# Kernel tuning notes

Hardware: AMD Instinct MI355X
Metric: run time of the kernel (lower is better)

## Reference

```python
import jax, jax.numpy as jnp
import numpy as np

B, S, DIM, HID, NE, TOPK = 2, 2048, 1024, 4096, 8, 2


def setup_inputs() -> dict:
    key = jax.random.key(0)
    ks = jax.random.split(key, 4)
    def init(k, shape, fan_in):
        return jax.random.normal(k, shape, jnp.float32) * (1.0 / np.sqrt(fan_in))
    return {
        "x": jax.random.normal(ks[0], (B, S, DIM), jnp.float32),
        "Wg": init(ks[1], (DIM, NE), DIM),
        "bg": jnp.zeros((NE,), jnp.float32),
        "W1": init(ks[2], (NE, DIM, HID), DIM),
        "b1": jnp.zeros((NE, HID), jnp.float32),
        "W2": init(ks[3], (NE, HID, DIM), HID),
        "b2": jnp.zeros((NE, DIM), jnp.float32),
        "top_k": TOPK,
    }


def reference(x, Wg, bg, W1, b1, W2, b2, top_k):
    Bx, Sx, D = x.shape
    T = Bx * Sx
    xt = x.reshape(T, D)                                   # [T, D] tokens
    # --- router: top-k softmax gating ---
    logits = xt @ Wg + bg                                  # [T, E]
    top_vals, top_idx = jax.lax.top_k(logits, top_k)       # [T, k]
    gate_w = jax.nn.softmax(top_vals, axis=-1)             # renormalized over chosen experts
    num_e = Wg.shape[1]
    # sparse combine weights: zero for non-selected experts
    w = jnp.zeros((T, num_e), xt.dtype).at[jnp.arange(T)[:, None], top_idx].set(gate_w)  # [T, E]
    # --- per-expert FFN (dense grouped-GEMM form) ---
    h = jax.nn.gelu(jnp.einsum('td,edh->eth', xt, W1) + b1[:, None, :])   # [E, T, H]
    y = jnp.einsum('eth,ehd->etd', h, W2) + b2[:, None, :]                # [E, T, D]
    moe_out = jnp.einsum('etd,te->td', y, w)                              # weighted combine
    # --- residual add (MoEBlock.forward: moe_out + skip; norm is unused) ---
    return (moe_out + xt).reshape(Bx, Sx, D)
```

## Files before the change

kernel.cpp:

```cpp
#include <hip/hip_runtime.h>

#define T_TOKENS 4096
#define DIM      1024
#define HID      4096
#define NE       8
#define TOPK     2
#define MAXTILES 72

typedef __attribute__((ext_vector_type(8))) short short8;
typedef __attribute__((ext_vector_type(4))) float f32x4;

__device__ __forceinline__ unsigned short f2bf(float f) {
    unsigned int u = __builtin_bit_cast(unsigned int, f);
    u += 0x7fffu + ((u >> 16) & 1u);
    return (unsigned short)(u >> 16);
}

__device__ __forceinline__ void gload16(const void* g, void* l) {
    __builtin_amdgcn_global_load_lds(
        (const __attribute__((address_space(1))) unsigned int*)g,
        (__attribute__((address_space(3))) unsigned int*)l, 16, 0, 0);
}

__global__ void router_kernel(const float* __restrict__ x, const float* __restrict__ Wg,
                              const float* __restrict__ bg, int* __restrict__ counts,
                              int* __restrict__ rowlist, float* __restrict__ gatelist) {
    const int wid  = threadIdx.x >> 6;
    const int lane = threadIdx.x & 63;
    const int t = blockIdx.x * 4 + wid;
    float acc[NE];
#pragma unroll
    for (int e = 0; e < NE; ++e) acc[e] = 0.f;
    const float* xr = x + (size_t)t * DIM;
    for (int d = lane; d < DIM; d += 64) {
        const float xv = xr[d];
        const float* wr = Wg + (size_t)d * NE;
#pragma unroll
        for (int e = 0; e < NE; ++e) acc[e] += xv * wr[e];
    }
#pragma unroll
    for (int off = 32; off > 0; off >>= 1) {
#pragma unroll
        for (int e = 0; e < NE; ++e) acc[e] += __shfl_xor(acc[e], off);
    }
    if (lane == 0) {
        float lg[NE];
#pragma unroll
        for (int e = 0; e < NE; ++e) lg[e] = acc[e] + bg[e];
        int i1 = 0; float v1 = lg[0];
#pragma unroll
        for (int e = 1; e < NE; ++e) if (lg[e] > v1) { v1 = lg[e]; i1 = e; }
        int i2 = -1; float v2 = -3.4e38f;
#pragma unroll
        for (int e = 0; e < NE; ++e) if (e != i1 && lg[e] > v2) { v2 = lg[e]; i2 = e; }
        const float ex = expf(v2 - v1);
        const float g1 = 1.f / (1.f + ex);
        const float g2 = ex / (1.f + ex);
        int p1 = atomicAdd(&counts[i1], 1);
        rowlist[i1 * T_TOKENS + p1] = t * 2;
        gatelist[i1 * T_TOKENS + p1] = g1;
        int p2 = atomicAdd(&counts[i2], 1);
        rowlist[i2 * T_TOKENS + p2] = t * 2 + 1;
        gatelist[i2 * T_TOKENS + p2] = g2;
    }
}

__global__ void planner_kernel(const int* __restrict__ counts, int* __restrict__ wl1,
                               int* __restrict__ wl2, int* __restrict__ nw) {
    __shared__ int tiles[NE], pref[NE + 1];
    const int tid = threadIdx.x;
    if (tid == 0) {
        int p = 0;
        for (int e = 0; e < NE; ++e) {
            tiles[e] = (counts[e] + 127) >> 7;
            pref[e] = p;
            p += tiles[e];
        }
        pref[NE] = p;
        nw[0] = p * 32;
        nw[1] = p * 16;
    }
    __syncthreads();
    const int n1 = pref[NE] * 32, n2 = pref[NE] * 16;
    for (int i = tid; i < n1; i += 256) {
        int e = 0;
        while (pref[e + 1] * 32 <= i) ++e;
        const int rel = i - pref[e] * 32;
        const int colt = rel / tiles[e];
        const int rt = rel - colt * tiles[e];
        wl1[i] = (e << 16) | (colt << 7) | rt;
    }
    for (int i = tid; i < n2; i += 256) {
        int e = 0;
        while (pref[e + 1] * 16 <= i) ++e;
        const int rel = i - pref[e] * 16;
        const int grp = rel / tiles[e];
        const int rt = rel - grp * tiles[e];
        wl2[i] = (e << 16) | ((grp >> 3) << 13) | ((grp & 7) << 7) | rt;
    }
}

__global__ void conv_bf16_kernel(const float* __restrict__ x, unsigned short* __restrict__ xb) {
    const int i = blockIdx.x * 256 + threadIdx.x;
    const float4 v = ((const float4*)x)[i];
    ushort4 o;
    o.x = f2bf(v.x); o.y = f2bf(v.y); o.z = f2bf(v.z); o.w = f2bf(v.w);
    ((ushort4*)xb)[i] = o;
}

__global__ void init_out_kernel(const float* __restrict__ x, float* __restrict__ out) {
    const int i = blockIdx.x * 256 + threadIdx.x;
    ((float4*)out)[i] = ((const float4*)x)[i];
}

template <int K, int N>
__global__ __launch_bounds__(256) void transconv_kernel(const float* __restrict__ W,
                                                        unsigned short* __restrict__ Wb) {
    const int e  = blockIdx.z;
    const int k0 = blockIdx.y * 64;
    const int nb = blockIdx.x * 64;
    __shared__ unsigned short t[64][72];
    const int tid = threadIdx.x;
    const int r  = tid >> 4;
    const int c4 = (tid & 15) * 4;
    const float* src = W + (size_t)e * K * N + (size_t)(k0 + r) * N + nb + c4;
#pragma unroll
    for (int p = 0; p < 4; ++p) {
        const float4 v = *(const float4*)(src + (size_t)p * 16 * N);
        ushort4 o;
        o.x = f2bf(v.x); o.y = f2bf(v.y); o.z = f2bf(v.z); o.w = f2bf(v.w);
        *(ushort4*)(&t[r + p * 16][c4]) = o;
    }
    __syncthreads();
#pragma unroll
    for (int p = 0; p < 4; ++p) {
        const int n  = (tid >> 4) + p * 16;
        const int kk = (tid & 15) * 4;
        ushort4 o;
        o.x = t[kk][n]; o.y = t[kk + 1][n]; o.z = t[kk + 2][n]; o.w = t[kk + 3][n];
        *(ushort4*)(Wb + (size_t)e * N * K + (size_t)(nb + n) * K + k0 + kk) = o;
    }
}

template <int PHASE, int SPLITK>
__global__ __launch_bounds__(256, 4) void moe_gemm(
    const unsigned short* __restrict__ A, const unsigned short* __restrict__ Wb,
    const float* __restrict__ bias, const int* __restrict__ counts,
    const int* __restrict__ rowlist, const float* __restrict__ gatelist,
    const int* __restrict__ wl, const int* __restrict__ nw,
    unsigned short* __restrict__ h, float* __restrict__ out) {
    constexpr int K = (PHASE == 1) ? DIM : HID;
    constexpr int N = (PHASE == 1) ? HID : DIM;
    constexpr int KC = K / SPLITK;
    constexpr int NT = KC / 64;
    const int nwork = nw[PHASE - 1];
    const int chunk = (nwork + 7) >> 3;
    const int pos = blockIdx.x >> 3;
    if (pos >= chunk) return;
    const int widx = (blockIdx.x & 7) * chunk + pos;
    if (widx >= nwork) return;
    const int w = wl[widx];
    const int e    = (w >> 16) & 7;
    const int kc   = (w >> 13) & 7;
    const int colt = (w >> 7) & 0x3f;
    const int rt   = w & 0x7f;
    const int cnt  = counts[e];
    const int n0   = colt * 128;

    __shared__ __align__(16) unsigned short As[128][64];
    __shared__ __align__(16) unsigned short Bs[128][64];
    __shared__ int rows_s[128];
    __shared__ float gates_s[128];

    const int tid = threadIdx.x;
    if (tid < 128) {
        const int gr = rt * 128 + tid;
        const int src = e * T_TOKENS + ((gr < cnt) ? gr : 0);
        rows_s[tid] = rowlist[src];
        gates_s[tid] = (gr < cnt) ? gatelist[src] : 0.f;
    }
    __syncthreads();

    const int lane = tid & 63;
    const int wv = tid >> 6;

    const int rowin = lane >> 3;
    const int kofs = ((lane & 7) ^ rowin) * 8;
    const unsigned short* sA[4];
    const unsigned short* sB[4];
    int dLds[4];
#pragma unroll
    for (int j = 0; j < 4; ++j) {
        const int r = (wv * 4 + j) * 8 + rowin;
        const int rid = rows_s[r];
        sA[j] = A + (size_t)((PHASE == 1) ? (rid >> 1) : rid) * K + kc * KC + kofs;
        sB[j] = Wb + (size_t)e * N * K + (size_t)(n0 + r) * K + kc * KC + kofs;
        dLds[j] = (wv * 4 + j) * 8 * 64;
    }

    const int wr = wv >> 1;
    const int wc = wv & 1;
    const int r15 = lane & 15;
    const int hi = lane >> 4;
    const int x7 = lane & 7;

    f32x4 acc[4][4];
#pragma unroll
    for (int m = 0; m < 4; ++m)
#pragma unroll
        for (int n = 0; n < 4; ++n)
#pragma unroll
            for (int r = 0; r < 4; ++r) acc[m][n][r] = 0.f;

    for (int t = 0; t < NT; ++t) {
        const int ko = t * 64;
#pragma unroll
        for (int j = 0; j < 4; ++j) gload16(sA[j] + ko, &As[0][0] + dLds[j]);
#pragma unroll
        for (int j = 0; j < 4; ++j) gload16(sB[j] + ko, &Bs[0][0] + dLds[j]);
        __syncthreads();

#pragma unroll
        for (int kk = 0; kk < 2; ++kk) {
            const int gsw = ((kk * 4 + hi) ^ x7) * 8;
            short8 af[4], bfr[4];
#pragma unroll
            for (int m = 0; m < 4; ++m)
                af[m] = *(const short8*)(&As[wr * 64 + m * 16 + r15][0] + gsw);
#pragma unroll
            for (int n = 0; n < 4; ++n)
                bfr[n] = *(const short8*)(&Bs[wc * 64 + n * 16 + r15][0] + gsw);
#pragma unroll
            for (int m = 0; m < 4; ++m)
#pragma unroll
                for (int n = 0; n < 4; ++n)
                    acc[m][n] = __builtin_amdgcn_mfma_f32_16x16x32_bf16(af[m], bfr[n], acc[m][n], 0, 0, 0);
        }
        __syncthreads();
    }

#pragma unroll
    for (int n = 0; n < 4; ++n) {
        const int col = n0 + wc * 64 + n * 16 + r15;
        const float bv = (PHASE == 1 || kc == 0) ? bias[(size_t)e * N + col] : 0.f;
#pragma unroll
        for (int m = 0; m < 4; ++m) {
            const int rbase = wr * 64 + m * 16 + hi * 4;
#pragma unroll
            for (int r = 0; r < 4; ++r) {
                const int row = rbase + r;
                if (rt * 128 + row < cnt) {
                    if (PHASE == 1) {
                        const float v = acc[m][n][r] + bv;
                        const float s = 1.f / (1.f + __expf(-1.5957691216f * (v + 0.044715f * v * v * v)));
                        h[(size_t)rows_s[row] * HID + col] = f2bf(v * s);
                    } else {
                        const float v = (acc[m][n][r] + bv) * gates_s[row];
                        atomicAdd(&out[(size_t)(rows_s[row] >> 1) * DIM + col], v);
                    }
                }
            }
        }
    }
}

extern "C" void kernel_launch(void* const* d_in, const int* in_sizes, int n_in,
                              void* d_out, int out_size, void* d_ws, size_t ws_size,
                              hipStream_t stream) {
    (void)in_sizes; (void)n_in; (void)out_size; (void)ws_size;
    const float* x  = (const float*)d_in[0];
    const float* Wg = (const float*)d_in[1];
    const float* bg = (const float*)d_in[2];
    const float* W1 = (const float*)d_in[3];
    const float* b1 = (const float*)d_in[4];
    const float* W2 = (const float*)d_in[5];
    const float* b2 = (const float*)d_in[6];
    float* out = (float*)d_out;

    char* ws = (char*)d_ws;
    size_t off = 0;
    auto alloc = [&](size_t bytes) -> void* {
        size_t a = (off + 255) & ~(size_t)255;
        off = a + bytes;
        return (void*)(ws + a);
    };
    int*   counts   = (int*)alloc(NE * sizeof(int));
    int*   nw       = (int*)alloc(2 * sizeof(int));
    int*   wl1      = (int*)alloc(MAXTILES * 32 * sizeof(int));
    int*   wl2      = (int*)alloc(MAXTILES * 16 * sizeof(int));
    int*   rowlist  = (int*)alloc((size_t)NE * T_TOKENS * sizeof(int));
    float* gatelist = (float*)alloc((size_t)NE * T_TOKENS * sizeof(float));
    unsigned short* xb  = (unsigned short*)alloc((size_t)T_TOKENS * DIM * 2);
    unsigned short* h   = (unsigned short*)alloc((size_t)T_TOKENS * TOPK * HID * 2);
    unsigned short* W1b = (unsigned short*)alloc((size_t)NE * DIM * HID * 2);
    unsigned short* W2b = (unsigned short*)alloc((size_t)NE * HID * DIM * 2);

    hipMemsetAsync(counts, 0, NE * sizeof(int), stream);
    router_kernel<<<T_TOKENS / 4, 256, 0, stream>>>(x, Wg, bg, counts, rowlist, gatelist);
    planner_kernel<<<1, 256, 0, stream>>>(counts, wl1, wl2, nw);
    const int nvec = T_TOKENS * DIM / 4;
    conv_bf16_kernel<<<nvec / 256, 256, 0, stream>>>(x, xb);
    init_out_kernel<<<nvec / 256, 256, 0, stream>>>(x, out);
    transconv_kernel<DIM, HID><<<dim3(HID / 64, DIM / 64, NE), 256, 0, stream>>>(W1, W1b);
    transconv_kernel<HID, DIM><<<dim3(DIM / 64, HID / 64, NE), 256, 0, stream>>>(W2, W2b);
    moe_gemm<1, 1><<<MAXTILES * 32, 256, 0, stream>>>(
        xb, W1b, b1, counts, rowlist, gatelist, wl1, nw, h, nullptr);
    moe_gemm<2, 2><<<MAXTILES * 16, 256, 0, stream>>>(
        h, W2b, b2, counts, rowlist, gatelist, wl2, nw, nullptr, out);
}
```

Baseline: 499.4 us.

## Shrink MoE GEMM tiles to 64x64, drop split-K, fuse conversion into router

Fuses the bf16 conversion of x and the residual initialization of the output into the router kernel, removing two elementwise launches. Reduces the grouped GEMM tile from 128x128 to 64x64 for both phases and removes split-K in the second GEMM, with the planner and work-list encoding updated to match. The aim is more blocks and higher occupancy, with less padding waste per expert. The cost is lower data reuse per tile, so more global and LDS traffic per MFMA.

```diff
diff --git a/kernel.cpp b/kernel.cpp
--- a/kernel.cpp
+++ b/kernel.cpp
@@ -5,7 +5,7 @@
 #define HID      4096
 #define NE       8
 #define TOPK     2
-#define MAXTILES 72
+#define MAXT64   136
 
 typedef __attribute__((ext_vector_type(8))) short short8;
 typedef __attribute__((ext_vector_type(4))) float f32x4;
@@ -22,9 +22,10 @@
         (__attribute__((address_space(3))) unsigned int*)l, 16, 0, 0);
 }
 
-__global__ void router_kernel(const float* __restrict__ x, const float* __restrict__ Wg,
-                              const float* __restrict__ bg, int* __restrict__ counts,
-                              int* __restrict__ rowlist, float* __restrict__ gatelist) {
+__global__ void prep_kernel(const float* __restrict__ x, const float* __restrict__ Wg,
+                            const float* __restrict__ bg, int* __restrict__ counts,
+                            int* __restrict__ rowlist, float* __restrict__ gatelist,
+                            unsigned short* __restrict__ xb, float* __restrict__ out) {
     const int wid  = threadIdx.x >> 6;
     const int lane = threadIdx.x & 63;
     const int t = blockIdx.x * 4 + wid;
@@ -63,6 +64,18 @@
         rowlist[i2 * T_TOKENS + p2] = t * 2 + 1;
         gatelist[i2 * T_TOKENS + p2] = g2;
     }
+    const float4* xr4 = (const float4*)xr;
+    float4* o4 = (float4*)(out + (size_t)t * DIM);
+    ushort4* xb4 = (ushort4*)(xb + (size_t)t * DIM);
+#pragma unroll
+    for (int p = 0; p < 4; ++p) {
+        const int i = p * 64 + lane;
+        const float4 v = xr4[i];
+        o4[i] = v;
+        ushort4 o;
+        o.x = f2bf(v.x); o.y = f2bf(v.y); o.z = f2bf(v.z); o.w = f2bf(v.w);
+        xb4[i] = o;
+    }
 }
 
 __global__ void planner_kernel(const int* __restrict__ counts, int* __restrict__ wl1,
@@ -72,45 +85,32 @@
     if (tid == 0) {
         int p = 0;
         for (int e = 0; e < NE; ++e) {
-            tiles[e] = (counts[e] + 127) >> 7;
+            tiles[e] = (counts[e] + 63) >> 6;
             pref[e] = p;
             p += tiles[e];
         }
         pref[NE] = p;
-        nw[0] = p * 32;
-        nw[1] = p * 16;
+        nw[0] = p * (HID / 64);
+        nw[1] = p * (DIM / 64);
     }
     __syncthreads();
-    const int n1 = pref[NE] * 32, n2 = pref[NE] * 16;
+    const int n1 = pref[NE] * (HID / 64), n2 = pref[NE] * (DIM / 64);
     for (int i = tid; i < n1; i += 256) {
         int e = 0;
-        while (pref[e + 1] * 32 <= i) ++e;
-        const int rel = i - pref[e] * 32;
+        while (pref[e + 1] * (HID / 64) <= i) ++e;
+        const int rel = i - pref[e] * (HID / 64);
         const int colt = rel / tiles[e];
         const int rt = rel - colt * tiles[e];
-        wl1[i] = (e << 16) | (colt << 7) | rt;
+        wl1[i] = (e << 20) | (colt << 8) | rt;
     }
     for (int i = tid; i < n2; i += 256) {
         int e = 0;
-        while (pref[e + 1] * 16 <= i) ++e;
-        const int rel = i - pref[e] * 16;
-        const int grp = rel / tiles[e];
-        const int rt = rel - grp * tiles[e];
-        wl2[i] = (e << 16) | ((grp >> 3) << 13) | ((grp & 7) << 7) | rt;
-    }
-}
-
-__global__ void conv_bf16_kernel(const float* __restrict__ x, unsigned short* __restrict__ xb) {
-    const int i = blockIdx.x * 256 + threadIdx.x;
-    const float4 v = ((const float4*)x)[i];
-    ushort4 o;
-    o.x = f2bf(v.x); o.y = f2bf(v.y); o.z = f2bf(v.z); o.w = f2bf(v.w);
-    ((ushort4*)xb)[i] = o;
-}
-
-__global__ void init_out_kernel(const float* __restrict__ x, float* __restrict__ out) {
-    const int i = blockIdx.x * 256 + threadIdx.x;
-    ((float4*)out)[i] = ((const float4*)x)[i];
+        while (pref[e + 1] * (DIM / 64) <= i) ++e;
+        const int rel = i - pref[e] * (DIM / 64);
+        const int colt = rel / tiles[e];
+        const int rt = rel - colt * tiles[e];
+        wl2[i] = (e << 20) | (colt << 8) | rt;
+    }
 }
 
 template <int K, int N>
@@ -142,8 +142,8 @@
     }
 }
 
-template <int PHASE, int SPLITK>
-__global__ __launch_bounds__(256, 4) void moe_gemm(
+template <int PHASE>
+__global__ __launch_bounds__(256, 6) void moe_gemm(
     const unsigned short* __restrict__ A, const unsigned short* __restrict__ Wb,
     const float* __restrict__ bias, const int* __restrict__ counts,
     const int* __restrict__ rowlist, const float* __restrict__ gatelist,
@@ -151,8 +151,7 @@
     unsigned short* __restrict__ h, float* __restrict__ out) {
     constexpr int K = (PHASE == 1) ? DIM : HID;
     constexpr int N = (PHASE == 1) ? HID : DIM;
-    constexpr int KC = K / SPLITK;
-    constexpr int NT = KC / 64;
+    constexpr int NT = K / 64;
     const int nwork = nw[PHASE - 1];
     const int chunk = (nwork + 7) >> 3;
     const int pos = blockIdx.x >> 3;
@@ -160,21 +159,20 @@
     const int widx = (blockIdx.x & 7) * chunk + pos;
     if (widx >= nwork) return;
     const int w = wl[widx];
-    const int e    = (w >> 16) & 7;
-    const int kc   = (w >> 13) & 7;
-    const int colt = (w >> 7) & 0x3f;
-    const int rt   = w & 0x7f;
+    const int e    = w >> 20;
+    const int colt = (w >> 8) & 0xfff;
+    const int rt   = w & 0xff;
     const int cnt  = counts[e];
-    const int n0   = colt * 128;
-
-    __shared__ __align__(16) unsigned short As[128][64];
-    __shared__ __align__(16) unsigned short Bs[128][64];
-    __shared__ int rows_s[128];
-    __shared__ float gates_s[128];
+    const int n0   = colt * 64;
+
+    __shared__ __align__(16) unsigned short As[64][64];
+    __shared__ __align__(16) unsigned short Bs[64][64];
+    __shared__ int rows_s[64];
+    __shared__ float gates_s[64];
 
     const int tid = threadIdx.x;
-    if (tid < 128) {
-        const int gr = rt * 128 + tid;
+    if (tid < 64) {
+        const int gr = rt * 64 + tid;
         const int src = e * T_TOKENS + ((gr < cnt) ? gr : 0);
         rows_s[tid] = rowlist[src];
         gates_s[tid] = (gr < cnt) ? gatelist[src] : 0.f;
@@ -186,16 +184,16 @@
 
     const int rowin = lane >> 3;
     const int kofs = ((lane & 7) ^ rowin) * 8;
-    const unsigned short* sA[4];
-    const unsigned short* sB[4];
-    int dLds[4];
-#pragma unroll
-    for (int j = 0; j < 4; ++j) {
-        const int r = (wv * 4 + j) * 8 + rowin;
+    const unsigned short* sA[2];
+    const unsigned short* sB[2];
+    int dLds[2];
+#pragma unroll
+    for (int j = 0; j < 2; ++j) {
+        const int r = (wv * 2 + j) * 8 + rowin;
         const int rid = rows_s[r];
-        sA[j] = A + (size_t)((PHASE == 1) ? (rid >> 1) : rid) * K + kc * KC + kofs;
-        sB[j] = Wb + (size_t)e * N * K + (size_t)(n0 + r) * K + kc * KC + kofs;
-        dLds[j] = (wv * 4 + j) * 8 * 64;
+        sA[j] = A + (size_t)((PHASE == 1) ? (rid >> 1) : rid) * K + kofs;
+        sB[j] = Wb + (size_t)e * N * K + (size_t)(n0 + r) * K + kofs;
+        dLds[j] = (wv * 2 + j) * 8 * 64;
     }
 
     const int wr = wv >> 1;
@@ -204,52 +202,52 @@
     const int hi = lane >> 4;
     const int x7 = lane & 7;
 
-    f32x4 acc[4][4];
-#pragma unroll
-    for (int m = 0; m < 4; ++m)
-#pragma unroll
-        for (int n = 0; n < 4; ++n)
+    f32x4 acc[2][2];
+#pragma unroll
+    for (int m = 0; m < 2; ++m)
+#pragma unroll
+        for (int n = 0; n < 2; ++n)
 #pragma unroll
             for (int r = 0; r < 4; ++r) acc[m][n][r] = 0.f;
 
     for (int t = 0; t < NT; ++t) {
         const int ko = t * 64;
 #pragma unroll
-        for (int j = 0; j < 4; ++j) gload16(sA[j] + ko, &As[0][0] + dLds[j]);
-#pragma unroll
-        for (int j = 0; j < 4; ++j) gload16(sB[j] + ko, &Bs[0][0] + dLds[j]);
+        for (int j = 0; j < 2; ++j) gload16(sA[j] + ko, &As[0][0] + dLds[j]);
+#pragma unroll
+        for (int j = 0; j < 2; ++j) gload16(sB[j] + ko, &Bs[0][0] + dLds[j]);
         __syncthreads();
 
 #pragma unroll
         for (int kk = 0; kk < 2; ++kk) {
             const int gsw = ((kk * 4 + hi) ^ x7) * 8;
-            short8 af[4], bfr[4];
-#pragma unroll
-            for (int m = 0; m < 4; ++m)
-                af[m] = *(const short8*)(&As[wr * 64 + m * 16 + r15][0] + gsw);
-#pragma unroll
-            for (int n = 0; n < 4; ++n)
-                bfr[n] = *(const short8*)(&Bs[wc * 64 + n * 16 + r15][0] + gsw);
-#pragma unroll
-            for (int m = 0; m < 4; ++m)
-#pragma unroll
-                for (int n = 0; n < 4; ++n)
+            short8 af[2], bfr[2];
+#pragma unroll
+            for (int m = 0; m < 2; ++m)
+                af[m] = *(const short8*)(&As[wr * 32 + m * 16 + r15][0] + gsw);
+#pragma unroll
+            for (int n = 0; n < 2; ++n)
+                bfr[n] = *(const short8*)(&Bs[wc * 32 + n * 16 + r15][0] + gsw);
+#pragma unroll
+            for (int m = 0; m < 2; ++m)
+#pragma unroll
+                for (int n = 0; n < 2; ++n)
                     acc[m][n] = __builtin_amdgcn_mfma_f32_16x16x32_bf16(af[m], bfr[n], acc[m][n], 0, 0, 0);
         }
         __syncthreads();
     }
 
 #pragma unroll
-    for (int n = 0; n < 4; ++n) {
-        const int col = n0 + wc * 64 + n * 16 + r15;
-        const float bv = (PHASE == 1 || kc == 0) ? bias[(size_t)e * N + col] : 0.f;
-#pragma unroll
-        for (int m = 0; m < 4; ++m) {
-            const int rbase = wr * 64 + m * 16 + hi * 4;
+    for (int n = 0; n < 2; ++n) {
+        const int col = n0 + wc * 32 + n * 16 + r15;
+        const float bv = bias[(size_t)e * N + col];
+#pragma unroll
+        for (int m = 0; m < 2; ++m) {
+            const int rbase = wr * 32 + m * 16 + hi * 4;
 #pragma unroll
             for (int r = 0; r < 4; ++r) {
                 const int row = rbase + r;
-                if (rt * 128 + row < cnt) {
+                if (rt * 64 + row < cnt) {
                     if (PHASE == 1) {
                         const float v = acc[m][n][r] + bv;
                         const float s = 1.f / (1.f + __expf(-1.5957691216f * (v + 0.044715f * v * v * v)));
@@ -286,8 +284,8 @@
     };
     int*   counts   = (int*)alloc(NE * sizeof(int));
     int*   nw       = (int*)alloc(2 * sizeof(int));
-    int*   wl1      = (int*)alloc(MAXTILES * 32 * sizeof(int));
-    int*   wl2      = (int*)alloc(MAXTILES * 16 * sizeof(int));
+    int*   wl1      = (int*)alloc((size_t)MAXT64 * (HID / 64) * sizeof(int));
+    int*   wl2      = (int*)alloc((size_t)MAXT64 * (DIM / 64) * sizeof(int));
     int*   rowlist  = (int*)alloc((size_t)NE * T_TOKENS * sizeof(int));
     float* gatelist = (float*)alloc((size_t)NE * T_TOKENS * sizeof(float));
     unsigned short* xb  = (unsigned short*)alloc((size_t)T_TOKENS * DIM * 2);
@@ -296,15 +294,12 @@
     unsigned short* W2b = (unsigned short*)alloc((size_t)NE * HID * DIM * 2);
 
     hipMemsetAsync(counts, 0, NE * sizeof(int), stream);
-    router_kernel<<<T_TOKENS / 4, 256, 0, stream>>>(x, Wg, bg, counts, rowlist, gatelist);
+    prep_kernel<<<T_TOKENS / 4, 256, 0, stream>>>(x, Wg, bg, counts, rowlist, gatelist, xb, out);
     planner_kernel<<<1, 256, 0, stream>>>(counts, wl1, wl2, nw);
-    const int nvec = T_TOKENS * DIM / 4;
-    conv_bf16_kernel<<<nvec / 256, 256, 0, stream>>>(x, xb);
-    init_out_kernel<<<nvec / 256, 256, 0, stream>>>(x, out);
     transconv_kernel<DIM, HID><<<dim3(HID / 64, DIM / 64, NE), 256, 0, stream>>>(W1, W1b);
     transconv_kernel<HID, DIM><<<dim3(DIM / 64, HID / 64, NE), 256, 0, stream>>>(W2, W2b);
-    moe_gemm<1, 1><<<MAXTILES * 32, 256, 0, stream>>>(
+    moe_gemm<1><<<MAXT64 * (HID / 64), 256, 0, stream>>>(
         xb, W1b, b1, counts, rowlist, gatelist, wl1, nw, h, nullptr);
-    moe_gemm<2, 2><<<MAXTILES * 16, 256, 0, stream>>>(
+    moe_gemm<2><<<MAXT64 * (DIM / 64), 256, 0, stream>>>(
         h, W2b, b2, counts, rowlist, gatelist, wl2, nw, nullptr, out);
 }
```

After: 506.8 us. Within noise of the previous version (+1.5%).

## Pipeline MoE GEMM with 4-stage LDS ring and fuse prep kernels

Applied to the files above, without the earlier changes.

Replaces the single-buffered 64-wide K loop in the grouped GEMM with a four-deep ring of 32-wide K stages. Async global-to-LDS loads run three stages ahead, gated by vmcnt waits and barriers, and MFMA issue priority is raised during compute. The bf16 conversion and output initialisation of x are folded into the router kernel, removing two launches and a second read of x. Occupancy hint drops to 2 blocks per CU because LDS use grows, and the work-item encoding is widened.

```diff
diff --git a/kernel.cpp b/kernel.cpp
--- a/kernel.cpp
+++ b/kernel.cpp
@@ -5,7 +5,7 @@
 #define HID      4096
 #define NE       8
 #define TOPK     2
-#define MAXTILES 72
+#define MAXT128  72
 
 typedef __attribute__((ext_vector_type(8))) short short8;
 typedef __attribute__((ext_vector_type(4))) float f32x4;
@@ -22,9 +22,17 @@
         (__attribute__((address_space(3))) unsigned int*)l, 16, 0, 0);
 }
 
-__global__ void router_kernel(const float* __restrict__ x, const float* __restrict__ Wg,
-                              const float* __restrict__ bg, int* __restrict__ counts,
-                              int* __restrict__ rowlist, float* __restrict__ gatelist) {
+#define PIPE_SYNC(N)                                            \
+    do {                                                        \
+        asm volatile("s_waitcnt vmcnt(" #N ")" ::: "memory");   \
+        __builtin_amdgcn_s_barrier();                           \
+        __builtin_amdgcn_sched_barrier(0);                      \
+    } while (0)
+
+__global__ void prep_kernel(const float* __restrict__ x, const float* __restrict__ Wg,
+                            const float* __restrict__ bg, int* __restrict__ counts,
+                            int* __restrict__ rowlist, float* __restrict__ gatelist,
+                            unsigned short* __restrict__ xb, float* __restrict__ out) {
     const int wid  = threadIdx.x >> 6;
     const int lane = threadIdx.x & 63;
     const int t = blockIdx.x * 4 + wid;
@@ -62,6 +70,18 @@
         int p2 = atomicAdd(&counts[i2], 1);
         rowlist[i2 * T_TOKENS + p2] = t * 2 + 1;
         gatelist[i2 * T_TOKENS + p2] = g2;
+    }
+    const float4* xr4 = (const float4*)xr;
+    float4* o4 = (float4*)(out + (size_t)t * DIM);
+    ushort4* xb4 = (ushort4*)(xb + (size_t)t * DIM);
+#pragma unroll
+    for (int p = 0; p < 4; ++p) {
+        const int i = p * 64 + lane;
+        const float4 v = xr4[i];
+        o4[i] = v;
+        ushort4 o;
+        o.x = f2bf(v.x); o.y = f2bf(v.y); o.z = f2bf(v.z); o.w = f2bf(v.w);
+        xb4[i] = o;
     }
 }
 
@@ -77,40 +97,27 @@
             p += tiles[e];
         }
         pref[NE] = p;
-        nw[0] = p * 32;
-        nw[1] = p * 16;
+        nw[0] = p * (HID / 128);
+        nw[1] = p * (DIM / 128) * 2;
     }
     __syncthreads();
-    const int n1 = pref[NE] * 32, n2 = pref[NE] * 16;
+    const int n1 = pref[NE] * (HID / 128), n2 = pref[NE] * (DIM / 128) * 2;
     for (int i = tid; i < n1; i += 256) {
         int e = 0;
-        while (pref[e + 1] * 32 <= i) ++e;
-        const int rel = i - pref[e] * 32;
+        while (pref[e + 1] * (HID / 128) <= i) ++e;
+        const int rel = i - pref[e] * (HID / 128);
         const int colt = rel / tiles[e];
         const int rt = rel - colt * tiles[e];
-        wl1[i] = (e << 16) | (colt << 7) | rt;
+        wl1[i] = (e << 24) | (colt << 8) | rt;
     }
     for (int i = tid; i < n2; i += 256) {
         int e = 0;
-        while (pref[e + 1] * 16 <= i) ++e;
-        const int rel = i - pref[e] * 16;
+        while (pref[e + 1] * (DIM / 128) * 2 <= i) ++e;
+        const int rel = i - pref[e] * (DIM / 128) * 2;
         const int grp = rel / tiles[e];
         const int rt = rel - grp * tiles[e];
-        wl2[i] = (e << 16) | ((grp >> 3) << 13) | ((grp & 7) << 7) | rt;
-    }
-}
-
-__global__ void conv_bf16_kernel(const float* __restrict__ x, unsigned short* __restrict__ xb) {
-    const int i = blockIdx.x * 256 + threadIdx.x;
-    const float4 v = ((const float4*)x)[i];
-    ushort4 o;
-    o.x = f2bf(v.x); o.y = f2bf(v.y); o.z = f2bf(v.z); o.w = f2bf(v.w);
-    ((ushort4*)xb)[i] = o;
-}
-
-__global__ void init_out_kernel(const float* __restrict__ x, float* __restrict__ out) {
-    const int i = blockIdx.x * 256 + threadIdx.x;
-    ((float4*)out)[i] = ((const float4*)x)[i];
+        wl2[i] = (e << 24) | ((grp >> 3) << 20) | ((grp & 7) << 8) | rt;
+    }
 }
 
 template <int K, int N>
@@ -143,7 +150,7 @@
 }
 
 template <int PHASE, int SPLITK>
-__global__ __launch_bounds__(256, 4) void moe_gemm(
+__global__ __launch_bounds__(256, 2) void moe_gemm(
     const unsigned short* __restrict__ A, const unsigned short* __restrict__ Wb,
     const float* __restrict__ bias, const int* __restrict__ counts,
     const int* __restrict__ rowlist, const float* __restrict__ gatelist,
@@ -152,7 +159,7 @@
     constexpr int K = (PHASE == 1) ? DIM : HID;
     constexpr int N = (PHASE == 1) ? HID : DIM;
     constexpr int KC = K / SPLITK;
-    constexpr int NT = KC / 64;
+    constexpr int NT = KC / 32;
     const int nwork = nw[PHASE - 1];
     const int chunk = (nwork + 7) >> 3;
     const int pos = blockIdx.x >> 3;
@@ -160,15 +167,15 @@
     const int widx = (blockIdx.x & 7) * chunk + pos;
     if (widx >= nwork) return;
     const int w = wl[widx];
-    const int e    = (w >> 16) & 7;
-    const int kc   = (w >> 13) & 7;
-    const int colt = (w >> 7) & 0x3f;
-    const int rt   = w & 0x7f;
+    const int e    = w >> 24;
+    const int kc   = (w >> 20) & 15;
+    const int colt = (w >> 8) & 0xfff;
+    const int rt   = w & 0xff;
     const int cnt  = counts[e];
     const int n0   = colt * 128;
 
-    __shared__ __align__(16) unsigned short As[128][64];
-    __shared__ __align__(16) unsigned short Bs[128][64];
+    __shared__ __align__(16) unsigned short As[4][128 * 32];
+    __shared__ __align__(16) unsigned short Bs[4][128 * 32];
     __shared__ int rows_s[128];
     __shared__ float gates_s[128];
 
@@ -184,25 +191,27 @@
     const int lane = tid & 63;
     const int wv = tid >> 6;
 
-    const int rowin = lane >> 3;
-    const int kofs = ((lane & 7) ^ rowin) * 8;
-    const unsigned short* sA[4];
-    const unsigned short* sB[4];
-    int dLds[4];
-#pragma unroll
-    for (int j = 0; j < 4; ++j) {
-        const int r = (wv * 4 + j) * 8 + rowin;
+    const int rowin = lane >> 2;
+    const int kofs = ((lane & 3) ^ (rowin & 3)) * 8;
+    const unsigned short* sA[2];
+    const unsigned short* sB[2];
+    int dLds[2];
+#pragma unroll
+    for (int j = 0; j < 2; ++j) {
+        const int r = (wv * 2 + j) * 16 + rowin;
         const int rid = rows_s[r];
         sA[j] = A + (size_t)((PHASE == 1) ? (rid >> 1) : rid) * K + kc * KC + kofs;
         sB[j] = Wb + (size_t)e * N * K + (size_t)(n0 + r) * K + kc * KC + kofs;
-        dLds[j] = (wv * 4 + j) * 8 * 64;
-    }
+        dLds[j] = (wv * 2 + j) * 16 * 32;
+    }
+    unsigned short* const aB = &As[0][0];
+    unsigned short* const bB = &Bs[0][0];
 
     const int wr = wv >> 1;
     const int wc = wv & 1;
     const int r15 = lane & 15;
     const int hi = lane >> 4;
-    const int x7 = lane & 7;
+    const int gsw = (hi ^ (lane & 3)) * 8;
 
     f32x4 acc[4][4];
 #pragma unroll
@@ -212,32 +221,44 @@
 #pragma unroll
             for (int r = 0; r < 4; ++r) acc[m][n][r] = 0.f;
 
-    for (int t = 0; t < NT; ++t) {
-        const int ko = t * 64;
-#pragma unroll
-        for (int j = 0; j < 4; ++j) gload16(sA[j] + ko, &As[0][0] + dLds[j]);
-#pragma unroll
-        for (int j = 0; j < 4; ++j) gload16(sB[j] + ko, &Bs[0][0] + dLds[j]);
-        __syncthreads();
-
-#pragma unroll
-        for (int kk = 0; kk < 2; ++kk) {
-            const int gsw = ((kk * 4 + hi) ^ x7) * 8;
-            short8 af[4], bfr[4];
-#pragma unroll
-            for (int m = 0; m < 4; ++m)
-                af[m] = *(const short8*)(&As[wr * 64 + m * 16 + r15][0] + gsw);
+    auto stage = [&](int t) {
+        const int ko = t * 32;
+        unsigned short* ab = aB + (t & 3) * 4096;
+        unsigned short* bb = bB + (t & 3) * 4096;
+#pragma unroll
+        for (int j = 0; j < 2; ++j) {
+            gload16(sA[j] + ko, ab + dLds[j]);
+            gload16(sB[j] + ko, bb + dLds[j]);
+        }
+    };
+    auto compute = [&](int t) {
+        const unsigned short* a = aB + (t & 3) * 4096;
+        const unsigned short* b = bB + (t & 3) * 4096;
+        short8 af[4], bfr[4];
+#pragma unroll
+        for (int m = 0; m < 4; ++m)
+            af[m] = *(const short8*)(a + (wr * 64 + m * 16 + r15) * 32 + gsw);
+#pragma unroll
+        for (int n = 0; n < 4; ++n)
+            bfr[n] = *(const short8*)(b + (wc * 64 + n * 16 + r15) * 32 + gsw);
+        __builtin_amdgcn_s_setprio(1);
+#pragma unroll
+        for (int m = 0; m < 4; ++m)
 #pragma unroll
             for (int n = 0; n < 4; ++n)
-                bfr[n] = *(const short8*)(&Bs[wc * 64 + n * 16 + r15][0] + gsw);
-#pragma unroll
-            for (int m = 0; m < 4; ++m)
-#pragma unroll
-                for (int n = 0; n < 4; ++n)
-                    acc[m][n] = __builtin_amdgcn_mfma_f32_16x16x32_bf16(af[m], bfr[n], acc[m][n], 0, 0, 0);
-        }
-        __syncthreads();
-    }
+                acc[m][n] = __builtin_amdgcn_mfma_f32_16x16x32_bf16(af[m], bfr[n], acc[m][n], 0, 0, 0);
+        __builtin_amdgcn_s_setprio(0);
+    };
+
+    stage(0); stage(1); stage(2);
+    for (int t = 0; t < NT - 3; ++t) {
+        PIPE_SYNC(8);
+        stage(t + 3);
+        compute(t);
+    }
+    PIPE_SYNC(8);  compute(NT - 3);
+    PIPE_SYNC(4);  compute(NT - 2);
+    PIPE_SYNC(0);  compute(NT - 1);
 
 #pragma unroll
     for (int n = 0; n < 4; ++n) {
@@ -286,8 +307,8 @@
     };
     int*   counts   = (int*)alloc(NE * sizeof(int));
     int*   nw       = (int*)alloc(2 * sizeof(int));
-    int*   wl1      = (int*)alloc(MAXTILES * 32 * sizeof(int));
-    int*   wl2      = (int*)alloc(MAXTILES * 16 * sizeof(int));
+    int*   wl1      = (int*)alloc((size_t)MAXT128 * (HID / 128) * sizeof(int));
+    int*   wl2      = (int*)alloc((size_t)MAXT128 * (DIM / 128) * 2 * sizeof(int));
     int*   rowlist  = (int*)alloc((size_t)NE * T_TOKENS * sizeof(int));
     float* gatelist = (float*)alloc((size_t)NE * T_TOKENS * sizeof(float));
     unsigned short* xb  = (unsigned short*)alloc((size_t)T_TOKENS * DIM * 2);
@@ -296,15 +317,12 @@
     unsigned short* W2b = (unsigned short*)alloc((size_t)NE * HID * DIM * 2);
 
     hipMemsetAsync(counts, 0, NE * sizeof(int), stream);
-    router_kernel<<<T_TOKENS / 4, 256, 0, stream>>>(x, Wg, bg, counts, rowlist, gatelist);
+    prep_kernel<<<T_TOKENS / 4, 256, 0, stream>>>(x, Wg, bg, counts, rowlist, gatelist, xb, out);
     planner_kernel<<<1, 256, 0, stream>>>(counts, wl1, wl2, nw);
-    const int nvec = T_TOKENS * DIM / 4;
-    conv_bf16_kernel<<<nvec / 256, 256, 0, stream>>>(x, xb);
-    init_out_kernel<<<nvec / 256, 256, 0, stream>>>(x, out);
     transconv_kernel<DIM, HID><<<dim3(HID / 64, DIM / 64, NE), 256, 0, stream>>>(W1, W1b);
     transconv_kernel<HID, DIM><<<dim3(DIM / 64, HID / 64, NE), 256, 0, stream>>>(W2, W2b);
-    moe_gemm<1, 1><<<MAXTILES * 32, 256, 0, stream>>>(
+    moe_gemm<1, 1><<<MAXT128 * (HID / 128), 256, 0, stream>>>(
         xb, W1b, b1, counts, rowlist, gatelist, wl1, nw, h, nullptr);
-    moe_gemm<2, 2><<<MAXTILES * 16, 256, 0, stream>>>(
+    moe_gemm<2, 2><<<MAXT128 * (DIM / 128) * 2, 256, 0, stream>>>(
         h, W2b, b2, counts, rowlist, gatelist, wl2, nw, nullptr, out);
 }
```

After: 625.7 us. 25.3% more time.

## Merge prep kernels and overlap weight transposes with router and GEMM1

Applied to the files above, without the earlier changes.

Folds the router, the x-to-bf16 conversion and the output init into a single prep body. The W1 transpose-convert runs as extra blocks of that same launch, and the W2 transpose-convert runs as extra blocks alongside GEMM1, cutting the launch count from 8 to 4. The goal is to fill idle CUs and overlap memory-bound weight conversion with compute. Weight loads now use nontemporal hints. The risk is that transconv blocks now share the GEMM kernel's launch bounds and shared-memory footprint, and that the heterogeneous blocks may not interleave as intended.

```diff
diff --git a/kernel.cpp b/kernel.cpp
--- a/kernel.cpp
+++ b/kernel.cpp
@@ -5,10 +5,17 @@
 #define HID      4096
 #define NE       8
 #define TOPK     2
-#define MAXTILES 72
+#define MAXT128  72
+
+#define PREP_BLOCKS (T_TOKENS / 4)
+#define TC_BLOCKS   (NE * (DIM / 64) * (HID / 64))
+#define G1_BLOCKS   (MAXT128 * 32)
+#define G2_BLOCKS   (MAXT128 * 16)
+#define SMEM_BYTES  33792
 
 typedef __attribute__((ext_vector_type(8))) short short8;
 typedef __attribute__((ext_vector_type(4))) float f32x4;
+typedef __attribute__((ext_vector_type(4))) unsigned short u16x4;
 
 __device__ __forceinline__ unsigned short f2bf(float f) {
     unsigned int u = __builtin_bit_cast(unsigned int, f);
@@ -22,12 +29,14 @@
         (__attribute__((address_space(3))) unsigned int*)l, 16, 0, 0);
 }
 
-__global__ void router_kernel(const float* __restrict__ x, const float* __restrict__ Wg,
-                              const float* __restrict__ bg, int* __restrict__ counts,
-                              int* __restrict__ rowlist, float* __restrict__ gatelist) {
+__device__ __forceinline__ void prep_body(
+    const float* __restrict__ x, const float* __restrict__ Wg,
+    const float* __restrict__ bg, int* __restrict__ counts,
+    int* __restrict__ rowlist, float* __restrict__ gatelist,
+    unsigned short* __restrict__ xb, float* __restrict__ out, int bid) {
     const int wid  = threadIdx.x >> 6;
     const int lane = threadIdx.x & 63;
-    const int t = blockIdx.x * 4 + wid;
+    const int t = bid * 4 + wid;
     float acc[NE];
 #pragma unroll
     for (int e = 0; e < NE; ++e) acc[e] = 0.f;
@@ -62,6 +71,48 @@
         int p2 = atomicAdd(&counts[i2], 1);
         rowlist[i2 * T_TOKENS + p2] = t * 2 + 1;
         gatelist[i2 * T_TOKENS + p2] = g2;
+    }
+    const float4* xr4 = (const float4*)xr;
+    float4* o4 = (float4*)(out + (size_t)t * DIM);
+    ushort4* xb4 = (ushort4*)(xb + (size_t)t * DIM);
+#pragma unroll
+    for (int p = 0; p < 4; ++p) {
+        const int i = p * 64 + lane;
+        const float4 v = xr4[i];
+        o4[i] = v;
+        ushort4 o;
+        o.x = f2bf(v.x); o.y = f2bf(v.y); o.z = f2bf(v.z); o.w = f2bf(v.w);
+        xb4[i] = o;
+    }
+}
+
+template <int K, int N>
+__device__ __forceinline__ void transconv_body(const float* __restrict__ W,
+                                               unsigned short* __restrict__ Wb,
+                                               int lin, char* smem) {
+    const int nb = (lin % (N / 64)) * 64;
+    const int k0 = ((lin / (N / 64)) % (K / 64)) * 64;
+    const int e  = lin / ((N / 64) * (K / 64));
+    unsigned short (*t)[72] = (unsigned short (*)[72])smem;
+    const int tid = threadIdx.x;
+    const int r  = tid >> 4;
+    const int c4 = (tid & 15) * 4;
+    const float* src = W + (size_t)e * K * N + (size_t)(k0 + r) * N + nb + c4;
+#pragma unroll
+    for (int p = 0; p < 4; ++p) {
+        const f32x4 v = __builtin_nontemporal_load((const f32x4*)(src + (size_t)p * 16 * N));
+        u16x4 o;
+        o.x = f2bf(v.x); o.y = f2bf(v.y); o.z = f2bf(v.z); o.w = f2bf(v.w);
+        *(u16x4*)(&t[r + p * 16][c4]) = o;
+    }
+    __syncthreads();
+#pragma unroll
+    for (int p = 0; p < 4; ++p) {
+        const int n  = (tid >> 4) + p * 16;
+        const int kk = (tid & 15) * 4;
+        u16x4 o;
+        o.x = t[kk][n]; o.y = t[kk + 1][n]; o.z = t[kk + 2][n]; o.w = t[kk + 3][n];
+        *(u16x4*)(Wb + (size_t)e * N * K + (size_t)(nb + n) * K + k0 + kk) = o;
     }
 }
 
@@ -100,64 +151,23 @@
     }
 }
 
-__global__ void conv_bf16_kernel(const float* __restrict__ x, unsigned short* __restrict__ xb) {
-    const int i = blockIdx.x * 256 + threadIdx.x;
-    const float4 v = ((const float4*)x)[i];
-    ushort4 o;
-    o.x = f2bf(v.x); o.y = f2bf(v.y); o.z = f2bf(v.z); o.w = f2bf(v.w);
-    ((ushort4*)xb)[i] = o;
-}
-
-__global__ void init_out_kernel(const float* __restrict__ x, float* __restrict__ out) {
-    const int i = blockIdx.x * 256 + threadIdx.x;
-    ((float4*)out)[i] = ((const float4*)x)[i];
-}
-
-template <int K, int N>
-__global__ __launch_bounds__(256) void transconv_kernel(const float* __restrict__ W,
-                                                        unsigned short* __restrict__ Wb) {
-    const int e  = blockIdx.z;
-    const int k0 = blockIdx.y * 64;
-    const int nb = blockIdx.x * 64;
-    __shared__ unsigned short t[64][72];
-    const int tid = threadIdx.x;
-    const int r  = tid >> 4;
-    const int c4 = (tid & 15) * 4;
-    const float* src = W + (size_t)e * K * N + (size_t)(k0 + r) * N + nb + c4;
-#pragma unroll
-    for (int p = 0; p < 4; ++p) {
-        const float4 v = *(const float4*)(src + (size_t)p * 16 * N);
-        ushort4 o;
-        o.x = f2bf(v.x); o.y = f2bf(v.y); o.z = f2bf(v.z); o.w = f2bf(v.w);
-        *(ushort4*)(&t[r + p * 16][c4]) = o;
-    }
-    __syncthreads();
-#pragma unroll
-    for (int p = 0; p < 4; ++p) {
-        const int n  = (tid >> 4) + p * 16;
-        const int kk = (tid & 15) * 4;
-        ushort4 o;
-        o.x = t[kk][n]; o.y = t[kk + 1][n]; o.z = t[kk + 2][n]; o.w = t[kk + 3][n];
-        *(ushort4*)(Wb + (size_t)e * N * K + (size_t)(nb + n) * K + k0 + kk) = o;
-    }
-}
-
 template <int PHASE, int SPLITK>
-__global__ __launch_bounds__(256, 4) void moe_gemm(
+__device__ __forceinline__ void gemm_body(
     const unsigned short* __restrict__ A, const unsigned short* __restrict__ Wb,
     const float* __restrict__ bias, const int* __restrict__ counts,
     const int* __restrict__ rowlist, const float* __restrict__ gatelist,
     const int* __restrict__ wl, const int* __restrict__ nw,
-    unsigned short* __restrict__ h, float* __restrict__ out) {
+    unsigned short* __restrict__ h, float* __restrict__ out,
+    int bid, int nblocks, char* smem) {
     constexpr int K = (PHASE == 1) ? DIM : HID;
     constexpr int N = (PHASE == 1) ? HID : DIM;
     constexpr int KC = K / SPLITK;
     constexpr int NT = KC / 64;
     const int nwork = nw[PHASE - 1];
     const int chunk = (nwork + 7) >> 3;
-    const int pos = blockIdx.x >> 3;
+    const int pos = bid >> 3;
     if (pos >= chunk) return;
-    const int widx = (blockIdx.x & 7) * chunk + pos;
+    const int widx = (bid & 7) * chunk + pos;
     if (widx >= nwork) return;
     const int w = wl[widx];
     const int e    = (w >> 16) & 7;
@@ -166,11 +176,12 @@
     const int rt   = w & 0x7f;
     const int cnt  = counts[e];
     const int n0   = colt * 128;
-
-    __shared__ __align__(16) unsigned short As[128][64];
-    __shared__ __align__(16) unsigned short Bs[128][64];
-    __shared__ int rows_s[128];
-    __shared__ float gates_s[128];
+    (void)nblocks;
+
+    unsigned short (*As)[64] = (unsigned short (*)[64])smem;
+    unsigned short (*Bs)[64] = (unsigned short (*)[64])(smem + 16384);
+    int*   rows_s  = (int*)(smem + 32768);
+    float* gates_s = (float*)(smem + 33280);
 
     const int tid = threadIdx.x;
     if (tid < 128) {
@@ -264,6 +275,45 @@
     }
 }
 
+__global__ __launch_bounds__(256, 4) void k1_prep_tc1(
+    const float* __restrict__ x, const float* __restrict__ Wg,
+    const float* __restrict__ bg, int* __restrict__ counts,
+    int* __restrict__ rowlist, float* __restrict__ gatelist,
+    unsigned short* __restrict__ xb, float* __restrict__ out,
+    const float* __restrict__ W1, unsigned short* __restrict__ W1b) {
+    __shared__ __align__(16) char smem[SMEM_BYTES];
+    if (blockIdx.x < PREP_BLOCKS)
+        prep_body(x, Wg, bg, counts, rowlist, gatelist, xb, out, blockIdx.x);
+    else
+        transconv_body<DIM, HID>(W1, W1b, blockIdx.x - PREP_BLOCKS, smem);
+}
+
+__global__ __launch_bounds__(256, 4) void k3_gemm1_tc2(
+    const unsigned short* __restrict__ xb, const unsigned short* __restrict__ W1b,
+    const float* __restrict__ b1, const int* __restrict__ counts,
+    const int* __restrict__ rowlist, const float* __restrict__ gatelist,
+    const int* __restrict__ wl1, const int* __restrict__ nw,
+    unsigned short* __restrict__ h,
+    const float* __restrict__ W2, unsigned short* __restrict__ W2b) {
+    __shared__ __align__(16) char smem[SMEM_BYTES];
+    if (blockIdx.x < G1_BLOCKS)
+        gemm_body<1, 1>(xb, W1b, b1, counts, rowlist, gatelist, wl1, nw,
+                        h, nullptr, blockIdx.x, G1_BLOCKS, smem);
+    else
+        transconv_body<HID, DIM>(W2, W2b, blockIdx.x - G1_BLOCKS, smem);
+}
+
+__global__ __launch_bounds__(256, 4) void k4_gemm2(
+    const unsigned short* __restrict__ h, const unsigned short* __restrict__ W2b,
+    const float* __restrict__ b2, const int* __restrict__ counts,
+    const int* __restrict__ rowlist, const float* __restrict__ gatelist,
+    const int* __restrict__ wl2, const int* __restrict__ nw,
+    float* __restrict__ out) {
+    __shared__ __align__(16) char smem[SMEM_BYTES];
+    gemm_body<2, 2>(h, W2b, b2, counts, rowlist, gatelist, wl2, nw,
+                    nullptr, out, blockIdx.x, G2_BLOCKS, smem);
+}
+
 extern "C" void kernel_launch(void* const* d_in, const int* in_sizes, int n_in,
                               void* d_out, int out_size, void* d_ws, size_t ws_size,
                               hipStream_t stream) {
@@ -286,8 +336,8 @@
     };
     int*   counts   = (int*)alloc(NE * sizeof(int));
     int*   nw       = (int*)alloc(2 * sizeof(int));
-    int*   wl1      = (int*)alloc(MAXTILES * 32 * sizeof(int));
-    int*   wl2      = (int*)alloc(MAXTILES * 16 * sizeof(int));
+    int*   wl1      = (int*)alloc((size_t)MAXT128 * 32 * sizeof(int));
+    int*   wl2      = (int*)alloc((size_t)MAXT128 * 16 * sizeof(int));
     int*   rowlist  = (int*)alloc((size_t)NE * T_TOKENS * sizeof(int));
     float* gatelist = (float*)alloc((size_t)NE * T_TOKENS * sizeof(float));
     unsigned short* xb  = (unsigned short*)alloc((size_t)T_TOKENS * DIM * 2);
@@ -296,15 +346,11 @@
     unsigned short* W2b = (unsigned short*)alloc((size_t)NE * HID * DIM * 2);
 
     hipMemsetAsync(counts, 0, NE * sizeof(int), stream);
-    router_kernel<<<T_TOKENS / 4, 256, 0, stream>>>(x, Wg, bg, counts, rowlist, gatelist);
+    k1_prep_tc1<<<PREP_BLOCKS + TC_BLOCKS, 256, 0, stream>>>(
+        x, Wg, bg, counts, rowlist, gatelist, xb, out, W1, W1b);
     planner_kernel<<<1, 256, 0, stream>>>(counts, wl1, wl2, nw);
-    const int nvec = T_TOKENS * DIM / 4;
-    conv_bf16_kernel<<<nvec / 256, 256, 0, stream>>>(x, xb);
-    init_out_kernel<<<nvec / 256, 256, 0, stream>>>(x, out);
-    transconv_kernel<DIM, HID><<<dim3(HID / 64, DIM / 64, NE), 256, 0, stream>>>(W1, W1b);
-    transconv_kernel<HID, DIM><<<dim3(DIM / 64, HID / 64, NE), 256, 0, stream>>>(W2, W2b);
-    moe_gemm<1, 1><<<MAXTILES * 32, 256, 0, stream>>>(
-        xb, W1b, b1, counts, rowlist, gatelist, wl1, nw, h, nullptr);
-    moe_gemm<2, 2><<<MAXTILES * 16, 256, 0, stream>>>(
-        h, W2b, b2, counts, rowlist, gatelist, wl2, nw, nullptr, out);
-}
+    k3_gemm1_tc2<<<G1_BLOCKS + TC_BLOCKS, 256, 0, stream>>>(
+        xb, W1b, b1, counts, rowlist, gatelist, wl1, nw, h, W2, W2b);
+    k4_gemm2<<<G2_BLOCKS, 256, 0, stream>>>(
+        h, W2b, b2, counts, rowlist, gatelist, wl2, nw, out);
+}
```

Result: faster. 421.3 us (-15.6%).
